# Optimization experiments

Measured on AMD Instinct MI355X. Metric: run time of the kernel, lower is better.

Reference implementation:

```python
import jax, jax.numpy as jnp
import numpy as np

ALPHA, NCLUST, LAMBD, GAMMA = 0.6, 3, 0.1, 0.01
KMEANS_ITERS = 10


def _conv(x, w, b):
    y = jax.lax.conv_general_dilated(x, w, (1, 1), 'SAME',
                                     dimension_numbers=('NCHW', 'OIHW', 'NCHW'))
    return y + b[None, :, None, None]


def _pool2(x):
    B, C, H, W = x.shape
    return x.reshape(B, C, H // 2, 2, W // 2, 2).mean(axis=(3, 5))


def _up2(x):
    return jnp.repeat(jnp.repeat(x, 2, axis=2), 2, axis=3)


def _encode(x, p, all_features=False):
    f1 = jax.nn.relu(_conv(x, p['e1_w'], p['e1_b']))
    f2 = jax.nn.relu(_conv(_pool2(f1), p['e2_w'], p['e2_b']))
    f3 = jax.nn.relu(_conv(_pool2(f2), p['e3_w'], p['e3_b']))
    f4 = jax.nn.relu(_conv(_pool2(f3), p['e4_w'], p['e4_b']))
    return (f1, f2, f3, f4) if all_features else f4


def _decode(f, p):
    x = jax.nn.relu(_conv(f, p['d1_w'], p['d1_b']))
    x = jax.nn.relu(_conv(_up2(x), p['d2_w'], p['d2_b']))
    x = jax.nn.relu(_conv(_up2(x), p['d3_w'], p['d3_b']))
    return _conv(_up2(x), p['d4_w'], p['d4_b'])


def _kmeans_onehot(pts, k):
    # pts: [N, C]; fixed-iteration Lloyd's, init = first k points.
    cent0 = pts[:k]

    def step(cent, _):
        d = ((pts[:, None, :] - cent[None]) ** 2).sum(-1)  # [N, K]
        oh = jax.nn.one_hot(jnp.argmin(d, axis=1), k, dtype=pts.dtype)
        cent = (oh.T @ pts) / (oh.sum(0)[:, None] + 1e-6)
        return cent, None

    cent, _ = jax.lax.scan(step, cent0, None, length=KMEANS_ITERS)
    d = ((pts[:, None, :] - cent[None]) ** 2).sum(-1)
    return jax.nn.one_hot(jnp.argmin(d, axis=1), k, dtype=pts.dtype)  # [N, K]


def _style_transfer(fc, fs):
    # fc, fs: [C, H, W] single-sample encoded features (original runs this per-sample on CPU numpy).
    C, H, W = fc.shape
    f = fc.reshape(C, -1)  # [C, N]
    s = fs.reshape(C, -1)  # [C, M]
    oh_c = _kmeans_onehot(f.T, NCLUST)  # [N, K]
    oh_s = _kmeans_onehot(s.T, NCLUST)  # [M, K]
    eye = LAMBD * jnp.eye(C, dtype=f.dtype)

    def cluster_T(wc, ws):
        # weighted whitening-coloring transform for one cluster pair
        nc = wc.sum() + 1e-6
        ns = ws.sum() + 1e-6
        mu_c = (f * wc).sum(1) / nc
        mu_s = (s * ws).sum(1) / ns
        fc_ = f - mu_c[:, None]
        fs_ = s - mu_s[:, None]
        cov_c = (fc_ * wc) @ fc_.T / nc + eye
        cov_s = (fs_ * ws) @ fs_.T / ns + eye
        lc, Ec = jnp.linalg.eigh(cov_c)
        ls, Es = jnp.linalg.eigh(cov_s)
        Wm = (Ec * jnp.clip(lc, 1e-6) ** -0.5) @ Ec.T  # whiten
        Cm = (Es * jnp.clip(ls, 1e-6) ** 0.5) @ Es.T   # color
        return Cm @ Wm, mu_c, mu_s

    Ts, mucs, muss = jax.vmap(cluster_T, in_axes=(1, 1))(oh_c, oh_s)  # [K,C,C],[K,C],[K,C]
    tpts = (jnp.einsum('kcd,dn->kcn', Ts, f)
            - jnp.einsum('kcd,kd->kc', Ts, mucs)[:, :, None]
            + muss[:, :, None])  # [K, C, N]
    fcs = jnp.einsum('nk,kcn->cn', oh_c, tpts)  # select per-point cluster transform
    return (ALPHA * fcs + (1.0 - ALPHA) * f).reshape(C, H, W)


def _forward(content_images, style_images, p):
    cf = _encode(content_images, p)
    sf = _encode(style_images, p)
    # original detaches to numpy -> no grad through the transfer
    tf_ = jax.lax.stop_gradient(jax.vmap(_style_transfer)(cf, sf))
    dec = _decode(tf_, p)
    ef = _encode(dec, p)
    all_ef = _encode(dec, p, all_features=True)
    all_sf = _encode(style_images, p, all_features=True)
    closs = jnp.mean((ef - cf) ** 2)
    sloss = 0.0
    for fa, fb in zip(all_ef, all_sf):
        sloss = sloss + jnp.mean((fa.mean((2, 3)) - fb.mean((2, 3))) ** 2)
        sloss = sloss + jnp.mean((fa.std((2, 3)) - fb.std((2, 3))) ** 2)
    return closs + GAMMA * sloss


PARAM_SHAPES = dict(
    e1_w=(64, 3, 3, 3), e1_b=(64,), e2_w=(128, 64, 3, 3), e2_b=(128,),
    e3_w=(256, 128, 3, 3), e3_b=(256,), e4_w=(512, 256, 3, 3), e4_b=(512,),
    d1_w=(256, 512, 3, 3), d1_b=(256,), d2_w=(128, 256, 3, 3), d2_b=(128,),
    d3_w=(64, 128, 3, 3), d3_b=(64,), d4_w=(3, 64, 3, 3), d4_b=(3,),
)


def setup_inputs() -> dict:
    key = jax.random.key(0)
    kc, ks, kp = jax.random.split(key, 3)
    inp = {
        'content_images': jax.random.uniform(kc, (4, 3, 256, 256), jnp.float32),
        'style_images': jax.random.uniform(ks, (4, 3, 256, 256), jnp.float32),
    }
    for i, (name, shp) in enumerate(PARAM_SHAPES.items()):
        fan_in = int(np.prod(shp[1:])) if len(shp) > 1 else 1
        inp[name] = jax.random.normal(jax.random.fold_in(kp, i), shp, jnp.float32) / np.sqrt(fan_in)
    return inp


def reference(content_images, style_images, e1_w, e1_b, e2_w, e2_b, e3_w, e3_b,
              e4_w, e4_b, d1_w, d1_b, d2_w, d2_b, d3_w, d3_b, d4_w, d4_b):
    p = dict(e1_w=e1_w, e1_b=e1_b, e2_w=e2_w, e2_b=e2_b, e3_w=e3_w, e3_b=e3_b,
             e4_w=e4_w, e4_b=e4_b, d1_w=d1_w, d1_b=d1_b, d2_w=d2_w, d2_b=d2_b,
             d3_w=d3_w, d3_b=d3_b, d4_w=d4_w, d4_b=d4_b)
    return _forward(content_images, style_images, p)
```

## Files before the change

kernel.cpp:

```cpp
#include <hip/hip_runtime.h>
#include <cstddef>

#define NS_ITERS 8
#define MSZ 262144
#define PL  6291456
#define KSLOT 12312

typedef unsigned short u16;
typedef __attribute__((ext_vector_type(8))) short bf16x8;
typedef __attribute__((ext_vector_type(4))) float f32x4;
typedef __attribute__((ext_vector_type(4))) short u16x4;

__device__ inline u16 bf16_rne(float x){
  unsigned u = __float_as_uint(x);
  unsigned r = u + 0x7fffu + ((u>>16)&1u);
  return (u16)(r>>16);
}
__device__ inline float bf16f(u16 h){
  return __uint_as_float(((unsigned)h)<<16);
}

#define OFF_F4C   0ul
#define OFF_F4S   2097152ul
#define OFF_TF    4194304ul
// ... 367 lines not shown
  const float* p = x + (size_t)bc*HW;
  double s = 0.0, s2 = 0.0;
  for (int i = tid; i < HW; i += 256){ double v = p[i]; s += v; s2 += v*v; }
  __shared__ double sh[256], sh2[256];
  sh[tid] = s; sh2[tid] = s2; __syncthreads();
  for (int k=128;k>0;k>>=1){ if (tid<k){ sh[tid]+=sh[tid+k]; sh2[tid]+=sh2[tid+k]; } __syncthreads(); }
  if (tid == 0){
    double m = sh[0]/HW;
    double var = sh2[0]/HW - m*m;
    if (var < 0.0) var = 0.0;
    mo[bc] = (float)m;
    so[bc] = (float)sqrt(var);
  }
}

__global__ __launch_bounds__(256) void transposek(const float* __restrict__ f4c,
                                                  const float* __restrict__ f4s,
                                                  float* __restrict__ ptsT){
  __shared__ float t[32][33];
  int r = blockIdx.z;
  const float* src = (r < 4) ? (f4c + (size_t)r*524288) : (f4s + (size_t)(r-4)*524288);
  int n0 = blockIdx.x*32, c0 = blockIdx.y*32;
  int lx = threadIdx.x & 31, ly = threadIdx.x >> 5;
  for (int j=0;j<32;j+=8)
    t[ly+j][lx] = src[(size_t)(c0+ly+j)*1024 + n0+lx];
  __syncthreads();
  for (int j=0;j<32;j+=8)
    ptsT[((size_t)r*1024 + n0+ly+j)*512 + c0+lx] = t[lx][ly+j];
}

__global__ __launch_bounds__(256) void initcent2k(const float* __restrict__ ptsT, float* __restrict__ KACC){
  int i = blockIdx.x*256 + threadIdx.x;
  if (i < 12288){
    int c = i & 511; int k = (i >> 9) % 3; int r = i / 1536;
    KACC[r*1536 + k*512 + c] = ptsT[((size_t)r*1024 + k)*512 + c];
  }
  if (i < 24) KACC[12288 + i] = 1.f;
}

__global__ __launch_bounds__(256) void kstepk(const float* __restrict__ ptsT,
    const float* __restrict__ prev, float* __restrict__ next,
    int* __restrict__ a, int nodiv)
{
  const int r = blockIdx.x, sl = blockIdx.y;
  const int tid = threadIdx.x;
  __shared__ float sc[1536];
  __shared__ int sa[32];
  __shared__ float red[3][8][32];
  __shared__ int scnt[3];
  if (tid < 3) scnt[tid] = 0;
  for (int i = tid; i < 1536; i += 256){
    float s = prev[r*1536 + i];
    float cnt = nodiv ? 1.f : (prev[12288 + r*3 + (i>>9)] + 1e-6f);
    sc[i] = s / cnt;
  }
  __syncthreads();
  const float* base = ptsT + (size_t)r*524288;
  const int wid = tid >> 6, lane = tid & 63;
  for (int rep = 0; rep < 8; ++rep){
    int p = wid*8 + rep;
    int n = sl*32 + p;
    const float* pp = base + (size_t)n*512;
    float d0=0.f,d1=0.f,d2=0.f;
    #pragma unroll
    for (int i=0;i<8;i++){
      int c = lane + i*64;
      float v = pp[c];
      float e0 = v - sc[c], e1 = v - sc[512+c], e2 = v - sc[1024+c];
      d0 = fmaf(e0,e0,d0); d1 = fmaf(e1,e1,d1); d2 = fmaf(e2,e2,d2);
    }
    #pragma unroll
    for (int off=32; off>0; off>>=1){
      d0 += __shfl_down(d0, off, 64);
      d1 += __shfl_down(d1, off, 64);
      d2 += __shfl_down(d2, off, 64);
    }
    if (lane == 0){
      int bi = 0; float bd = d0;
      if (d1 < bd){ bd = d1; bi = 1; }
      if (d2 < bd){ bd = d2; bi = 2; }
      sa[p] = bi;
      a[r*1024 + n] = bi;
    }
  }
  __syncthreads();
  if (tid < 32) atomicAdd(&scnt[sa[tid]], 1);
  __syncthreads();
  if (tid < 3) atomicAdd(&next[12288 + r*3 + tid], (float)scnt[tid]);
  const int g = tid >> 5, lc = tid & 31;
  for (int cj = 0; cj < 16; ++cj){
    int c = cj*32 + lc;
    float s0=0.f,s1=0.f,s2=0.f;
    #pragma unroll
    for (int q=0;q<4;q++){
      int nl = g*4 + q;
      float v = base[(size_t)(sl*32+nl)*512 + c];
      int an = sa[nl];
      s0 += (an==0)?v:0.f;
      s1 += (an==1)?v:0.f;
      s2 += (an==2)?v:0.f;
    }
    red[0][g][lc]=s0; red[1][g][lc]=s1; red[2][g][lc]=s2;
    __syncthreads();
    if (g == 0){
      float t0=0.f,t1=0.f,t2=0.f;
      #pragma unroll
      for (int q2=0;q2<8;q2++){ t0+=red[0][q2][lc]; t1+=red[1][q2][lc]; t2+=red[2][q2][lc]; }
      atomicAdd(&next[r*1536 +          c], t0);
      atomicAdd(&next[r*1536 +  512 +   c], t1);
      atomicAdd(&next[r*1536 + 1024 +   c], t2);
    }
    __syncthreads();
  }
}

__global__ __launch_bounds__(256) void mufink(const float* __restrict__ slot,
                                              float* __restrict__ mu, float* __restrict__ counts){
  int i = blockIdx.x*256 + threadIdx.x;
  if (i >= 12288) return;
  int c = i & 511; int k = (i >> 9) % 3; int r = i / 1536;
  int cs = r >> 2, img = r & 3;
  int i0 = cs*12 + img*3;
  float cnt = slot[12288 + r*3 + k];
  mu[(size_t)(i0+k)*512 + c] = slot[r*1536 + k*512 + c] / (cnt + 1e-6f);
  if (c == 0) counts[i0+k] = cnt;
}

__global__ __launch_bounds__(256) void maskcenterk(const float* __restrict__ f4c, const float* __restrict__ f4s,
        const int* __restrict__ a, const float* __restrict__ mu,
        u16* __restrict__ Ph, u16* __restrict__ Pl){
  size_t i4 = ((size_t)blockIdx.x*256 + threadIdx.x)*4;
  if (i4 >= (size_t)PL*2) return;
  int z = (int)(i4 >> 19);
  int rc = (int)(i4 & 524287);
  int c = rc >> 10, n = rc & 1023;
  int cs = z / 12; int rem = z - cs*12; int img = rem / 3; int k = rem - img*3;
  const float* pts = (cs ? f4s : f4c) + (size_t)img*524288;
  float m = mu[(size_t)z*512 + c];
  const int* an = a + (cs*4 + img)*1024 + n;
  float4 v4 = *(const float4*)&pts[(size_t)c*1024 + n];
  float vv[4] = {v4.x, v4.y, v4.z, v4.w};
  u16x4 oh, ol;
  #pragma unroll
  for (int j=0;j<4;j++){
    float v = (an[j] == k) ? (vv[j] - m) : 0.f;
    u16 h = bf16_rne(v);
    oh[j] = (short)h;
    ol[j] = (short)bf16_rne(v - bf16f(h));
  }
  *(u16x4*)&Ph[i4] = oh;
  *(u16x4*)&Pl[i4] = ol;
}

__global__ __launch_bounds__(256) void covgemm(const u16* __restrict__ Ph, const u16* __restrict__ Pl,
        const float* __restrict__ counts, float* __restrict__ Ycov, float* __restrict__ trsum){
  const int z = blockIdx.z;
  const u16* Pbh = Ph + (size_t)z*524288;
  const u16* Pbl = Pl + (size_t)z*524288;
  const int m0 = blockIdx.y*128, n0 = blockIdx.x*128;
  const int tid = threadIdx.x;

  __shared__ __align__(16) u16 sAh[128*40], sAl[128*40];
  __shared__ __align__(16) u16 sBh[128*40], sBl[128*40];

  const int ra = tid >> 2, qa = tid & 3;
  const int wid = tid >> 6, lane = tid & 63;
  const int wm = wid >> 1, wn = wid & 1;
  const int quad = lane >> 4, ln = lane & 15;

  f32x4 acc[4][4];
  #pragma unroll
  for (int i=0;i<4;i++)
    #pragma unroll
    for (int j=0;j<4;j++)
      #pragma unroll
      for (int e=0;e<4;e++) acc[i][j][e] = 0.f;

  for (int k0 = 0; k0 < 1024; k0 += 32){
    *(bf16x8*)&sAh[ra*40 + qa*8]      = *(const bf16x8*)&Pbh[(size_t)(m0+ra)*1024    + k0 + qa*8];
    *(bf16x8*)&sAl[ra*40 + qa*8]      = *(const bf16x8*)&Pbl[(size_t)(m0+ra)*1024    + k0 + qa*8];
    *(bf16x8*)&sAh[(ra+64)*40 + qa*8] = *(const bf16x8*)&Pbh[(size_t)(m0+ra+64)*1024 + k0 + qa*8];
    *(bf16x8*)&sAl[(ra+64)*40 + qa*8] = *(const bf16x8*)&Pbl[(size_t)(m0+ra+64)*1024 + k0 + qa*8];
    *(bf16x8*)&sBh[ra*40 + qa*8]      = *(const bf16x8*)&Pbh[(size_t)(n0+ra)*1024    + k0 + qa*8];
    *(bf16x8*)&sBl[ra*40 + qa*8]      = *(const bf16x8*)&Pbl[(size_t)(n0+ra)*1024    + k0 + qa*8];
    *(bf16x8*)&sBh[(ra+64)*40 + qa*8] = *(const bf16x8*)&Pbh[(size_t)(n0+ra+64)*1024 + k0 + qa*8];
    *(bf16x8*)&sBl[(ra+64)*40 + qa*8] = *(const bf16x8*)&Pbl[(size_t)(n0+ra+64)*1024 + k0 + qa*8];
    __syncthreads();

    bf16x8 ah[4], al[4], bh[4], bl[4];
    #pragma unroll
    for (int t=0;t<4;t++){
      const int moA = ((wm*4+t)*16 + ln)*40 + quad*8;
      const int moB = ((wn*4+t)*16 + ln)*40 + quad*8;
      ah[t] = *(const bf16x8*)&sAh[moA];
      al[t] = *(const bf16x8*)&sAl[moA];
      bh[t] = *(const bf16x8*)&sBh[moB];
      bl[t] = *(const bf16x8*)&sBl[moB];
    }
    #pragma unroll
    for (int mi=0;mi<4;mi++)
      #pragma unroll
      for (int ni=0;ni<4;ni++){
        acc[mi][ni] = __builtin_amdgcn_mfma_f32_16x16x32_bf16(ah[mi], bh[ni], acc[mi][ni], 0, 0, 0);
        acc[mi][ni] = __builtin_amdgcn_mfma_f32_16x16x32_bf16(ah[mi], bl[ni], acc[mi][ni], 0, 0, 0);
        acc[mi][ni] = __builtin_amdgcn_mfma_f32_16x16x32_bf16(al[mi], bh[ni], acc[mi][ni], 0, 0, 0);
      }
    __syncthreads();
  }
  const float inv = 1.f/(counts[z] + 1e-6f);
  float dsum = 0.f; bool anyd = false;
  #pragma unroll
  for (int mi=0;mi<4;mi++){
    const int mbase = m0 + (wm*4+mi)*16 + quad*4;
    #pragma unroll
    for (int ni=0;ni<4;ni++){
      const int n = n0 + (wn*4+ni)*16 + ln;
      #pragma unroll
      for (int rg=0;rg<4;rg++){
        const int m = mbase + rg;
        float v = acc[mi][ni][rg]*inv + ((m==n)?0.1f:0.f);
        Ycov[(size_t)z*MSZ + (size_t)m*512 + n] = v;
        if (m0==n0 && m==n){ dsum += v; anyd = true; }
      }
    }
  }
  if (anyd) atomicAdd(&trsum[z], dsum);
}

__global__ __launch_bounds__(256) void nsinitk(const float* __restrict__ Ycov, const float* __restrict__ sval,
                                               u16* __restrict__ Yh, u16* __restrict__ Yl,
                                               u16* __restrict__ Zh, u16* __restrict__ Zl){
  size_t idx = (size_t)blockIdx.x*256 + threadIdx.x;
  if (idx >= (size_t)PL) return;
  int z = (int)(idx >> 18);
  int rc = (int)(idx & (MSZ-1));
  int rr = rc >> 9, cc = rc & 511;
  float y = Ycov[idx] / sval[z];
  u16 h = bf16_rne(y);
  Yh[idx] = h;
  Yl[idx] = bf16_rne(y - bf16f(h));
  Zh[idx] = (rr==cc) ? (u16)0x3F80 : (u16)0;
  Zl[idx] = 0;
}

template<int MODE, int SYMB>
__global__ __launch_bounds__(256) void bmms(
    const u16* __restrict__ Ah, const u16* __restrict__ Al,
    const u16* __restrict__ Bh, const u16* __restrict__ Bl,
    u16* __restrict__ Ch, u16* __restrict__ Cl,
    const float* __restrict__ osc,
    int aoff, float* __restrict__ trAcc)
{
  const int z = blockIdx.z;
  const u16* Abh = Ah + (size_t)(z+aoff)*MSZ;
  const u16* Abl = Al + (size_t)(z+aoff)*MSZ;
  const u16* Bbh = Bh + (size_t)z*MSZ;
  const u16* Bbl = Bl + (size_t)z*MSZ;
  const int m0 = blockIdx.y*128, n0 = blockIdx.x*128;
  const int tid = threadIdx.x;

  __shared__ __align__(16) u16 sAh[128*40], sAl[128*40];
  __shared__ __align__(16) u16 sBh[128*40], sBl[128*40];

  const int ra = tid >> 2, qa = tid & 3;
  const int kb = tid >> 4, gb = tid & 15;

  const int wid = tid >> 6, lane = tid & 63;
  const int wm = wid >> 1, wn = wid & 1;
  const int quad = lane >> 4, ln = lane & 15;

  f32x4 acc[4][4];
  #pragma unroll
  for (int i=0;i<4;i++)
    #pragma unroll
    for (int j=0;j<4;j++)
      #pragma unroll
      for (int e=0;e<4;e++) acc[i][j][e] = 0.f;

  for (int k0 = 0; k0 < 512; k0 += 32){
    *(bf16x8*)&sAh[ra*40 + qa*8]      = *(const bf16x8*)&Abh[(size_t)(m0+ra)*512    + k0 + qa*8];
    *(bf16x8*)&sAl[ra*40 + qa*8]      = *(const bf16x8*)&Abl[(size_t)(m0+ra)*512    + k0 + qa*8];
    *(bf16x8*)&sAh[(ra+64)*40 + qa*8] = *(const bf16x8*)&Abh[(size_t)(m0+ra+64)*512 + k0 + qa*8];
    *(bf16x8*)&sAl[(ra+64)*40 + qa*8] = *(const bf16x8*)&Abl[(size_t)(m0+ra+64)*512 + k0 + qa*8];
    if constexpr (SYMB){
      *(bf16x8*)&sBh[ra*40 + qa*8]      = *(const bf16x8*)&Bbh[(size_t)(n0+ra)*512    + k0 + qa*8];
      *(bf16x8*)&sBl[ra*40 + qa*8]      = *(const bf16x8*)&Bbl[(size_t)(n0+ra)*512    + k0 + qa*8];
      *(bf16x8*)&sBh[(ra+64)*40 + qa*8] = *(const bf16x8*)&Bbh[(size_t)(n0+ra+64)*512 + k0 + qa*8];
      *(bf16x8*)&sBl[(ra+64)*40 + qa*8] = *(const bf16x8*)&Bbl[(size_t)(n0+ra+64)*512 + k0 + qa*8];
    } else {
      bf16x8 vh = *(const bf16x8*)&Bbh[(size_t)(k0+kb)*512 + n0 + gb*8];
      bf16x8 vl = *(const bf16x8*)&Bbl[(size_t)(k0+kb)*512 + n0 + gb*8];
      #pragma unroll
      for (int j=0;j<8;j++){
        sBh[(gb*8+j)*40 + kb] = (u16)vh[j];
        sBl[(gb*8+j)*40 + kb] = (u16)vl[j];
      }
      vh = *(const bf16x8*)&Bbh[(size_t)(k0+kb+16)*512 + n0 + gb*8];
      vl = *(const bf16x8*)&Bbl[(size_t)(k0+kb+16)*512 + n0 + gb*8];
      #pragma unroll
      for (int j=0;j<8;j++){
        sBh[(gb*8+j)*40 + kb+16] = (u16)vh[j];
        sBl[(gb*8+j)*40 + kb+16] = (u16)vl[j];
      }
    }
    __syncthreads();

    bf16x8 ah[4], al[4], bh[4], bl[4];
    #pragma unroll
    for (int t=0;t<4;t++){
      const int moA = ((wm*4+t)*16 + ln)*40 + quad*8;
      const int moB = ((wn*4+t)*16 + ln)*40 + quad*8;
      ah[t] = *(const bf16x8*)&sAh[moA];
      al[t] = *(const bf16x8*)&sAl[moA];
      bh[t] = *(const bf16x8*)&sBh[moB];
      bl[t] = *(const bf16x8*)&sBl[moB];
    }
    #pragma unroll
    for (int mi=0;mi<4;mi++)
      #pragma unroll
      for (int ni=0;ni<4;ni++){
        acc[mi][ni] = __builtin_amdgcn_mfma_f32_16x16x32_bf16(ah[mi], bh[ni], acc[mi][ni], 0, 0, 0);
        acc[mi][ni] = __builtin_amdgcn_mfma_f32_16x16x32_bf16(ah[mi], bl[ni], acc[mi][ni], 0, 0, 0);
        acc[mi][ni] = __builtin_amdgcn_mfma_f32_16x16x32_bf16(al[mi], bh[ni], acc[mi][ni], 0, 0, 0);
      }
    __syncthreads();
  }

  float alpha = 1.f;
  if constexpr (MODE==2){ alpha = osc[z]; }

  float dsum = 0.f; bool anyd = false;
  #pragma unroll
  for (int mi=0;mi<4;mi++){
    const int mbase = m0 + (wm*4+mi)*16 + quad*4;
    #pragma unroll
    for (int ni=0;ni<4;ni++){
      const int n = n0 + (wn*4+ni)*16 + ln;
      #pragma unroll
      for (int rg=0;rg<4;rg++){
        const int m = mbase + rg;
        const size_t off = (size_t)z*MSZ + (size_t)m*512 + n;
        float v = alpha*acc[mi][ni][rg];
        u16 h = bf16_rne(v);
        Ch[off] = h;
        Cl[off] = bf16_rne(v - bf16f(h));
        if (MODE==0 && trAcc && m0==n0 && m==n){ dsum += v; anyd = true; }
      }
    }
  }
  if (MODE==0 && anyd) atomicAdd(&trAcc[z], dsum);
}

__global__ __launch_bounds__(256) void bmmpair(
    const u16* __restrict__ Yh, const u16* __restrict__ Yl,
    const u16* __restrict__ Mh, const u16* __restrict__ Ml,
    const u16* __restrict__ Zh, const u16* __restrict__ Zl,
    u16* __restrict__ Y2h, u16* __restrict__ Y2l,
    u16* __restrict__ Z2h, u16* __restrict__ Z2l,
    const float* __restrict__ trAcc, int last)
{
  const int z = blockIdx.z;
  int zz; bool isY;
  if (last){ zz = z; isY = (z >= 12); }
  else { isY = (z < 24); zz = isY ? z : (z - 24); }
  const size_t zo = (size_t)zz*MSZ;
  const u16 *Abh, *Abl, *Bbh, *Bbl, *Dbh, *Dbl;
  u16 *Cbh, *Cbl;
  if (isY){
    Abh = Yh + zo; Abl = Yl + zo;
    Bbh = Mh + zo; Bbl = Ml + zo;
    Dbh = Yh + zo; Dbl = Yl + zo;
    Cbh = Y2h + zo; Cbl = Y2l + zo;
  } else {
    Abh = Mh + zo; Abl = Ml + zo;
    Bbh = Zh + zo; Bbl = Zl + zo;
    Dbh = Zh + zo; Dbl = Zl + zo;
    Cbh = Z2h + zo; Cbl = Z2l + zo;
  }
  const int m0 = blockIdx.y*128, n0 = blockIdx.x*128;
  const int tid = threadIdx.x;

  __shared__ __align__(16) u16 sAh[128*40], sAl[128*40];
  __shared__ __align__(16) u16 sBh[128*40], sBl[128*40];

  const int ra = tid >> 2, qa = tid & 3;
  const int wid = tid >> 6, lane = tid & 63;
  const int wm = wid >> 1, wn = wid & 1;
  const int quad = lane >> 4, ln = lane & 15;

  f32x4 acc[4][4];
  #pragma unroll
  for (int i=0;i<4;i++)
    #pragma unroll
    for (int j=0;j<4;j++)
      #pragma unroll
      for (int e=0;e<4;e++) acc[i][j][e] = 0.f;

  for (int k0 = 0; k0 < 512; k0 += 32){
    *(bf16x8*)&sAh[ra*40 + qa*8]      = *(const bf16x8*)&Abh[(size_t)(m0+ra)*512    + k0 + qa*8];
    *(bf16x8*)&sAl[ra*40 + qa*8]      = *(const bf16x8*)&Abl[(size_t)(m0+ra)*512    + k0 + qa*8];
    *(bf16x8*)&sAh[(ra+64)*40 + qa*8] = *(const bf16x8*)&Abh[(size_t)(m0+ra+64)*512 + k0 + qa*8];
    *(bf16x8*)&sAl[(ra+64)*40 + qa*8] = *(const bf16x8*)&Abl[(size_t)(m0+ra+64)*512 + k0 + qa*8];
    *(bf16x8*)&sBh[ra*40 + qa*8]      = *(const bf16x8*)&Bbh[(size_t)(n0+ra)*512    + k0 + qa*8];
    *(bf16x8*)&sBl[ra*40 + qa*8]      = *(const bf16x8*)&Bbl[(size_t)(n0+ra)*512    + k0 + qa*8];
    *(bf16x8*)&sBh[(ra+64)*40 + qa*8] = *(const bf16x8*)&Bbh[(size_t)(n0+ra+64)*512 + k0 + qa*8];
    *(bf16x8*)&sBl[(ra+64)*40 + qa*8] = *(const bf16x8*)&Bbl[(size_t)(n0+ra+64)*512 + k0 + qa*8];
    __syncthreads();

    bf16x8 ah[4], al[4], bh[4], bl[4];
    #pragma unroll
    for (int t=0;t<4;t++){
      const int moA = ((wm*4+t)*16 + ln)*40 + quad*8;
      const int moB = ((wn*4+t)*16 + ln)*40 + quad*8;
      ah[t] = *(const bf16x8*)&sAh[moA];
      al[t] = *(const bf16x8*)&sAl[moA];
      bh[t] = *(const bf16x8*)&sBh[moB];
      bl[t] = *(const bf16x8*)&sBl[moB];
    }
    #pragma unroll
    for (int mi=0;mi<4;mi++)
      #pragma unroll
      for (int ni=0;ni<4;ni++){
        acc[mi][ni] = __builtin_amdgcn_mfma_f32_16x16x32_bf16(ah[mi], bh[ni], acc[mi][ni], 0, 0, 0);
        acc[mi][ni] = __builtin_amdgcn_mfma_f32_16x16x32_bf16(ah[mi], bl[ni], acc[mi][ni], 0, 0, 0);
        acc[mi][ni] = __builtin_amdgcn_mfma_f32_16x16x32_bf16(al[mi], bh[ni], acc[mi][ni], 0, 0, 0);
      }
    __syncthreads();
  }

  const float tr = trAcc[zz];
  const float g2 = fminf(512.f/fmaxf(tr, 1e-6f), 2.7f);
  const float oz = 0.5f*sqrtf(g2);
  const float alpha = -g2*oz, beta = 3.f*oz;

  #pragma unroll
  for (int mi=0;mi<4;mi++){
    const int mbase = m0 + (wm*4+mi)*16 + quad*4;
    #pragma unroll
    for (int ni=0;ni<4;ni++){
      const int n = n0 + (wn*4+ni)*16 + ln;
      #pragma unroll
      for (int rg=0;rg<4;rg++){
        const int m = mbase + rg;
        const size_t off = (size_t)m*512 + n;
        float v = alpha*acc[mi][ni][rg] + beta*(bf16f(Dbh[off]) + bf16f(Dbl[off]));
        u16 h = bf16_rne(v);
        Cbh[off] = h;
        Cbl[off] = bf16_rne(v - bf16f(h));
      }
    }
  }
}

__global__ __launch_bounds__(256) void bmmt(
    const u16* __restrict__ Th, const u16* __restrict__ Tl,
    const u16* __restrict__ fh, const u16* __restrict__ fl,
    float* __restrict__ Cf)
{
  const int z = blockIdx.z;
  const u16* Abh = Th + (size_t)z*MSZ;
  const u16* Abl = Tl + (size_t)z*MSZ;
  const u16* Bbh = fh + (size_t)(z/3)*524288;
  const u16* Bbl = fl + (size_t)(z/3)*524288;
  const int m0 = blockIdx.y*128, n0 = blockIdx.x*128;
  const int tid = threadIdx.x;

  __shared__ __align__(16) u16 sAh[128*40], sAl[128*40];
  __shared__ __align__(16) u16 sBh[128*40], sBl[128*40];

  const int ra = tid >> 2, qa = tid & 3;
  const int kb = tid >> 4, gb = tid & 15;
  const int wid = tid >> 6, lane = tid & 63;
  const int wm = wid >> 1, wn = wid & 1;
  const int quad = lane >> 4, ln = lane & 15;

  f32x4 acc[4][4];
  #pragma unroll
  for (int i=0;i<4;i++)
    #pragma unroll
    for (int j=0;j<4;j++)
      #pragma unroll
      for (int e=0;e<4;e++) acc[i][j][e] = 0.f;

  for (int k0 = 0; k0 < 512; k0 += 32){
    *(bf16x8*)&sAh[ra*40 + qa*8]      = *(const bf16x8*)&Abh[(size_t)(m0+ra)*512    + k0 + qa*8];
    *(bf16x8*)&sAl[ra*40 + qa*8]      = *(const bf16x8*)&Abl[(size_t)(m0+ra)*512    + k0 + qa*8];
    *(bf16x8*)&sAh[(ra+64)*40 + qa*8] = *(const bf16x8*)&Abh[(size_t)(m0+ra+64)*512 + k0 + qa*8];
    *(bf16x8*)&sAl[(ra+64)*40 + qa*8] = *(const bf16x8*)&Abl[(size_t)(m0+ra+64)*512 + k0 + qa*8];
    {
      bf16x8 vh = *(const bf16x8*)&Bbh[(size_t)(k0+kb)*1024 + n0 + gb*8];
      bf16x8 vl = *(const bf16x8*)&Bbl[(size_t)(k0+kb)*1024 + n0 + gb*8];
      #pragma unroll
      for (int j=0;j<8;j++){
        sBh[(gb*8+j)*40 + kb] = (u16)vh[j];
        sBl[(gb*8+j)*40 + kb] = (u16)vl[j];
      }
      vh = *(const bf16x8*)&Bbh[(size_t)(k0+kb+16)*1024 + n0 + gb*8];
      vl = *(const bf16x8*)&Bbl[(size_t)(k0+kb+16)*1024 + n0 + gb*8];
      #pragma unroll
      for (int j=0;j<8;j++){
        sBh[(gb*8+j)*40 + kb+16] = (u16)vh[j];
        sBl[(gb*8+j)*40 + kb+16] = (u16)vl[j];
      }
    }
    __syncthreads();

    bf16x8 ah[4], al[4], bh[4], bl[4];
    #pragma unroll
    for (int t=0;t<4;t++){
      const int moA = ((wm*4+t)*16 + ln)*40 + quad*8;
      const int moB = ((wn*4+t)*16 + ln)*40 + quad*8;
      ah[t] = *(const bf16x8*)&sAh[moA];
      al[t] = *(const bf16x8*)&sAl[moA];
      bh[t] = *(const bf16x8*)&sBh[moB];
      bl[t] = *(const bf16x8*)&sBl[moB];
    }
    #pragma unroll
    for (int mi=0;mi<4;mi++)
      #pragma unroll
      for (int ni=0;ni<4;ni++){
        acc[mi][ni] = __builtin_amdgcn_mfma_f32_16x16x32_bf16(ah[mi], bh[ni], acc[mi][ni], 0, 0, 0);
        acc[mi][ni] = __builtin_amdgcn_mfma_f32_16x16x32_bf16(ah[mi], bl[ni], acc[mi][ni], 0, 0, 0);
        acc[mi][ni] = __builtin_amdgcn_mfma_f32_16x16x32_bf16(al[mi], bh[ni], acc[mi][ni], 0, 0, 0);
      }
    __syncthreads();
  }
  #pragma unroll
  for (int mi=0;mi<4;mi++){
    const int mbase = m0 + (wm*4+mi)*16 + quad*4;
    #pragma unroll
    for (int ni=0;ni<4;ni++){
      const int n = n0 + (wn*4+ni)*16 + ln;
      #pragma unroll
      for (int rg=0;rg<4;rg++){
        const int m = mbase + rg;
        Cf[(size_t)z*524288 + (size_t)m*1024 + n] = acc[mi][ni][rg];
      }
    }
  }
}

__global__ __launch_bounds__(256) void splitk(const float* __restrict__ src,
                                              u16* __restrict__ dh, u16* __restrict__ dl, int n4){
  int i = blockIdx.x*256 + threadIdx.x;
  if (i >= n4) return;
  float4 v4 = *(const float4*)&src[(size_t)i*4];
  float vv[4] = {v4.x, v4.y, v4.z, v4.w};
  u16x4 oh, ol;
  #pragma unroll
  for (int j=0;j<4;j++){
    u16 h = bf16_rne(vv[j]);
    oh[j] = (short)h;
    ol[j] = (short)bf16_rne(vv[j] - bf16f(h));
  }
  *(u16x4*)&dh[(size_t)i*4] = oh;
  *(u16x4*)&dl[(size_t)i*4] = ol;
}

__global__ void make_scalesk(const float* __restrict__ sval, float* __restrict__ scl){
  int i = threadIdx.x;
  if (i < 12) scl[i] = sqrtf(sval[12+i] / sval[i]);
}

__global__ __launch_bounds__(512) void tveck(const u16* __restrict__ Th, const u16* __restrict__ Tl,
                                             const float* __restrict__ mu, float* __restrict__ tvec){
  int b = blockIdx.x; int c = threadIdx.x;
  __shared__ float mc[512];
  mc[c] = mu[(size_t)b*512 + c];
  __syncthreads();
  const u16* Trh = Th + ((size_t)b*512 + c)*512;
  const u16* Trl = Tl + ((size_t)b*512 + c)*512;
  float s = 0.f;
  for (int d=0; d<512; d++) s = fmaf(bf16f(Trh[d]) + bf16f(Trl[d]), mc[d], s);
  tvec[b*512 + c] = mu[(size_t)(12+b)*512 + c] - s;
}

__global__ __launch_bounds__(256) void selectk(const float* __restrict__ tpts, const float* __restrict__ tvec,
        const int* __restrict__ a, const float* __restrict__ f4c, float* __restrict__ tf){
  size_t idx = (size_t)blockIdx.x*256 + threadIdx.x;
  if (idx >= 2097152ul) return;
  int n = (int)(idx & 1023);
  int c = (int)((idx >> 10) & 511);
  int img = (int)(idx >> 19);
  int k = a[img*1024 + n];
  int b = img*3 + k;
  float v = tpts[((size_t)b*512 + c)*1024 + n] + tvec[b*512 + c];
  tf[idx] = 0.6f*v + 0.4f*f4c[idx];
}

__global__ __launch_bounds__(256) void clossk(const float* __restrict__ x, const float* __restrict__ y,
                                              int n, float* __restrict__ acc){
  int tid = threadIdx.x;
  float s = 0.f;
  for (size_t i = (size_t)blockIdx.x*256 + tid; i < (size_t)n; i += (size_t)gridDim.x*256){
    float d = x[i] - y[i]; s = fmaf(d, d, s);
  }
  __shared__ float sh[256];
  sh[tid] = s; __syncthreads();
  for (int k=128;k>0;k>>=1){ if (tid<k) sh[tid]+=sh[tid+k]; __syncthreads(); }
  if (tid==0) atomicAdd(acc, sh[0]);
}

__global__ __launch_bounds__(256) void finalk(const float* __restrict__ sm, float* __restrict__ out){
  int tid = threadIdx.x;
  const int cnts[4] = {256,512,1024,2048};
  const int offs[4] = {0,256,768,1792};
  const float* mS = sm + SM_STATS_S;
  const float* sS = sm + SM_STATS_S + 3840;
  const float* mD = sm + SM_STATS_D;
  const float* sD = sm + SM_STATS_D + 3840;
  double sl = 0.0;
  for (int L=0; L<4; ++L){
    int cnt = cnts[L], off = offs[L];
    double inv = 1.0/cnt;
    for (int i=tid; i<cnt; i+=256){
      double dm = (double)mD[off+i] - (double)mS[off+i];
      double ds = (double)sD[off+i] - (double)sS[off+i];
      sl += (dm*dm + ds*ds)*inv;
    }
  }
  __shared__ double sh[256];
  sh[tid] = sl; __syncthreads();
  for (int k=128;k>0;k>>=1){ if (tid<k) sh[tid]+=sh[tid+k]; __syncthreads(); }
  if (tid==0){
    double closs = (double)sm[SM_CLOSS] / 2097152.0;
    out[0] = (float)(closs + 0.01*sh[0]);
  }
}


extern "C" void kernel_launch(void* const* d_in, const int* in_sizes, int n_in,
                              void* d_out, int out_size, void* d_ws, size_t ws_size,
                              hipStream_t stream)
{
  const float* content = (const float*)d_in[0];
  const float* style   = (const float*)d_in[1];
  const float* Wm[8]; const float* Bm[8];
  for (int i=0;i<8;i++){ Wm[i] = (const float*)d_in[2+2*i]; Bm[i] = (const float*)d_in[3+2*i]; }
  float* out = (float*)d_out;
  float* ws = (float*)d_ws;

  float* f4c  = ws + OFF_F4C;
  float* f4s  = ws + OFF_F4S;
  float* tf   = ws + OFF_TF;
  float* dec  = ws + OFF_DEC;
  float* sm   = ws + OFF_SMALL;
  float* AR   = ws + OFF_ARENA;
  int*   aPtr = (int*)(sm + SM_ASSIGN);
  float* mu   = sm + SM_MU;
  float* counts = sm + SM_COUNTS;
  float* sval = sm + SM_SVAL;
  float* scl  = sm + SM_SCALE;
  float* tvec = sm + SM_TVEC;
  float* trbuf = sm + SM_TR;

  u16* WB = (u16*)(ws + OFF_WSPL);
  u16 *w2h=WB+0,       *w2l=WB+73728;
  u16 *w3h=WB+147456,  *w3l=WB+442368;
  u16 *w4h=WB+737280,  *w4l=WB+1916928;
  u16 *v1h=WB+3096576, *v1l=WB+4276224;
  u16 *v2h=WB+5455872, *v2l=WB+5750784;
  u16 *v3h=WB+6045696, *v3l=WB+6119424;

  float* Ycov = AR;
  u16* Mh  = (u16*)(AR);
  u16* Ml  = (u16*)(AR + 3145728ul);
  u16* Yh  = (u16*)(AR + 6291456ul);
  u16* Yl  = (u16*)(AR + 9437184ul);
  u16* Zh  = (u16*)(AR + 12582912ul);
  u16* Zl  = (u16*)(AR + 15728640ul);
  u16* Y2h = (u16*)(AR + 18874368ul);
  u16* Y2l = (u16*)(AR + 22020096ul);
  u16* Z2h = (u16*)(AR + 25165824ul);
  u16* Z2l = (u16*)(AR + 28311552ul);
  u16* Ph  = (u16*)(AR + 18874368ul);
  u16* Pl  = (u16*)(AR + 25165824ul);
  float* ptsT = AR + 25165824ul;
  u16* Th  = (u16*)(AR + 18874368ul);
  u16* Tl  = (u16*)(AR + 20971520ul);
  u16* fsh = (u16*)(AR + 23068672ul);
  u16* fsl = (u16*)(AR + 24117248ul);
  float* KACC = AR + 0;

  u16* xP1h  = (u16*)(AR + 16777216ul);
  u16* xP1l  = (u16*)(AR + 20971520ul);
  u16* xF2ph = (u16*)(AR + 16777216ul);
  u16* xF2pl = (u16*)(AR + 18874368ul);
  u16* xF3ph = (u16*)(AR + 18874368ul);
  u16* xF3pl = (u16*)(AR + 19922944ul);
  u16* xTFh  = (u16*)(AR + 8388608ul);
  u16* xTFl  = (u16*)(AR + 9437184ul);
  u16* xX1h  = (u16*)(AR + 1048576ul);
  u16* xX1l  = (u16*)(AR + 1572864ul);
  u16* xX2h  = (u16*)(AR + 11534336ul);
  u16* xX2l  = (u16*)(AR + 12582912ul);
  u16* xP1dh = (u16*)(AR + 16777216ul);
  u16* xP1dl = (u16*)(AR + 18874368ul);
  u16* xF2dph= (u16*)(AR + 16777216ul);
  u16* xF2dpl= (u16*)(AR + 17825792ul);
  u16* xF3dph= (u16*)(AR + 16777216ul);
  u16* xF3dpl= (u16*)(AR + 17301504ul);

  zerok<<<512,256,0,stream>>>(sm, 131072);

  {
    auto wsp = [&](int li, u16* wh, u16* wl, int Co, int Ci){
      int n = 9*Co*Ci;
      wsplitk<<<(n+255)/256,256,0,stream>>>(Wm[li], wh, wl, Co, Ci);
    };
    wsp(1,w2h,w2l,128,64);
    wsp(2,w3h,w3l,256,128);
    wsp(3,w4h,w4l,512,256);
    wsp(4,v1h,v1l,256,512);
    wsp(5,v2h,v2l,128,256);
    wsp(6,v3h,v3l,64,128);
  }

  auto convMFMA = [&](const u16* xh, const u16* xl, int li, float* outp,
                      int B,int Ci,int Co,int H,int Wd,int relu,int KS,int RZ,float* part){
    const u16 *wh=nullptr,*wl=nullptr;
    switch(li){
      case 1: wh=w2h; wl=w2l; break;
      case 2: wh=w3h; wl=w3l; break;
      case 3: wh=w4h; wl=w4l; break;
      case 4: wh=v1h; wl=v1l; break;
      case 5: wh=v2h; wl=v2l; break;
      case 6: wh=v3h; wl=v3l; break;
    }
    int tiles = (H>>3)*(Wd>>4);
    if (KS==1){
      dim3 g(tiles,Co>>6,B);
      if (RZ==0) convm<1,0><<<g,256,0,stream>>>(xh,xl,wh,wl,Bm[li],outp,Ci,Co,H,Wd,relu);
      else       convm<1,2><<<g,256,0,stream>>>(xh,xl,wh,wl,Bm[li],outp,Ci,Co,H,Wd,relu);
    } else if (KS==2){
      dim3 g(tiles,Co>>6,B*2);
      if (RZ==0) convm<2,0><<<g,256,0,stream>>>(xh,xl,wh,wl,nullptr,part,Ci,Co,H,Wd,relu);
      else       convm<2,2><<<g,256,0,stream>>>(xh,xl,wh,wl,nullptr,part,Ci,Co,H,Wd,relu);
      int n = B*Co*H*Wd;
      sumk<<<(n+255)/256,256,0,stream>>>(part,Bm[li],outp,Co,H*Wd,2,relu,n);
    } else {
      dim3 g(tiles,Co>>6,B*4);
      convm<4,0><<<g,256,0,stream>>>(xh,xl,wh,wl,nullptr,part,Ci,Co,H,Wd,relu);
      int n = B*Co*H*Wd;
      sumk<<<(n+255)/256,256,0,stream>>>(part,Bm[li],outp,Co,H*Wd,4,relu,n);
    }
  };

  float* mS = sm + SM_STATS_S;
  float* sS = sm + SM_STATS_S + 3840;

  float* F1   = AR + 0;
  float* F2_8 = AR + 0;
  float* F3_8 = AR + 0;
  float* PART8 = AR + 10485760ul;

  {
    dim3 ge(64, 8, 4);
    conv3x3<8,4,1,0,0><<<ge,256,0,stream>>>(content,Wm[0],Bm[0],F1,xP1h,           xP1l,           4,3,64,256,256,1);
    conv3x3<8,4,1,1,0><<<ge,256,0,stream>>>(style,  Wm[0],Bm[0],F1,xP1h+4194304ul, xP1l+4194304ul, 4,3,64,256,256,1);
  }
  statsk<<<256,256,0,stream>>>(F1,65536, mS+0, sS+0);

  convMFMA(xP1h,xP1l, 1, F2_8, 8, 64,128,128,128,1,1,0,nullptr);
  statsk<<<512,256,0,stream>>>(F2_8 + 8388608ul, 16384, mS+256, sS+256);
  repackk<1><<<dim3(128,2,8),256,0,stream>>>(F2_8, xF2ph, xF2pl, 128,64,64);
  convMFMA(xF2ph,xF2pl, 2, F3_8, 8, 128,256,64,64,1,1,0,nullptr);
  statsk<<<1024,256,0,stream>>>(F3_8 + 4194304ul, 4096, mS+768, sS+768);
  repackk<1><<<dim3(32,4,8),256,0,stream>>>(F3_8, xF3ph, xF3pl, 256,32,32);
  convMFMA(xF3ph,xF3pl, 3, f4c, 8, 256,512,32,32,1,2,0,PART8);
  statsk<<<2048,256,0,stream>>>(f4s,1024, mS+1792, sS+1792);

  transposek<<<dim3(32,16,8),256,0,stream>>>(f4c,f4s,ptsT);
  zerok<<<(12*KSLOT+255)/256,256,0,stream>>>(KACC, 12*KSLOT);
  initcent2k<<<48,256,0,stream>>>(ptsT,KACC);
  for (int it=0; it<=10; ++it){
    kstepk<<<dim3(8,32),256,0,stream>>>(ptsT, KACC + (size_t)it*KSLOT, KACC + (size_t)(it+1)*KSLOT, aPtr, it==0 ? 1 : 0);
  }
  mufink<<<48,256,0,stream>>>(KACC + 11ul*KSLOT, mu, counts);

  maskcenterk<<<12288,256,0,stream>>>(f4c,f4s,aPtr,mu,Ph,Pl);
  covgemm<<<dim3(4,4,24),256,0,stream>>>(Ph,Pl,counts,Ycov,sval);
  nsinitk<<<24576,256,0,stream>>>(Ycov,sval,Yh,Yl,Zh,Zl);

  u16 *Ych=Yh,*Ycl=Yl,*Zch=Zh,*Zcl=Zl,*Yah=Y2h,*Yal=Y2l,*Zah=Z2h,*Zal=Z2l;
  for (int it=0; it<NS_ITERS; ++it){
    bmms<0,1><<<dim3(4,4,24),256,0,stream>>>(Zch,Zcl,Ych,Ycl,Mh,Ml,nullptr,0,trbuf+it*24);
    if (it < NS_ITERS-1)
      bmmpair<<<dim3(4,4,48),256,0,stream>>>(Ych,Ycl,Mh,Ml,Zch,Zcl,Yah,Yal,Zah,Zal,trbuf+it*24,0);
    else
      bmmpair<<<dim3(4,4,24),256,0,stream>>>(Ych,Ycl,Mh,Ml,Zch,Zcl,Yah,Yal,Zah,Zal,trbuf+it*24,1);
    u16* t;
    t=Ych;Ych=Yah;Yah=t; t=Ycl;Ycl=Yal;Yal=t;
    t=Zch;Zch=Zah;Zah=t; t=Zcl;Zcl=Zal;Zal=t;
  }
  make_scalesk<<<1,64,0,stream>>>(sval,scl);
  bmms<2,1><<<dim3(4,4,12),256,0,stream>>>(Ych,Ycl,Zch,Zcl,Th,Tl,scl,12,nullptr);
  tveck<<<12,512,0,stream>>>(Th,Tl,mu,tvec);
  splitk<<<2048,256,0,stream>>>(f4c,fsh,fsl,524288);
  float* Mb = AR + 0;
  bmmt<<<dim3(8,4,12),256,0,stream>>>(Th,Tl,fsh,fsl,Mb);
  selectk<<<8192,256,0,stream>>>(Mb,tvec,aPtr,f4c,tf);

  float* X1 = AR + 0;
  float* X2 = AR + 5242880ul;
  float* X3 = AR + 0;
  float* PARTA = AR + 2097152ul;
  float* PARTB = AR + 7340032ul;
  repackk<0><<<dim3(32,8,4),256,0,stream>>>(tf, xTFh, xTFl, 512,32,32);
  convMFMA(xTFh,xTFl, 4, X1, 4, 512,256,32,32,1,4,0,PARTA);
  repackk<0><<<dim3(32,4,4),256,0,stream>>>(X1, xX1h, xX1l, 256,32,32);
  convMFMA(xX1h,xX1l, 5, X2, 4, 256,128,64,64,1,2,2,PARTB);
  repackk<0><<<dim3(128,2,4),256,0,stream>>>(X2, xX2h, xX2l, 128,64,64);
  convMFMA(xX2h,xX2l, 6, X3, 4, 128,64,128,128,1,1,2,nullptr);
  d4upk<<<dim3(256,1,4),256,0,stream>>>(X3, Wm[7], Bm[7], dec);

  float* mD = sm + SM_STATS_D;
  float* sD = sm + SM_STATS_D + 3840;
  float* F1d = AR + 0;
  float* F2d = AR + 0;
  float* F3d = AR + 10485760ul;
  {
    dim3 ge(64, 8, 4);
    conv3x3<8,4,1,1,0><<<ge,256,0,stream>>>(dec,Wm[0],Bm[0],F1d,xP1dh,xP1dl,4,3,64,256,256,1);
  }
  statsk<<<256,256,0,stream>>>(F1d,65536, mD+0, sD+0);
  convMFMA(xP1dh,xP1dl, 1, F2d, 4, 64,128,128,128,1,1,0,nullptr);
  statsk<<<512,256,0,stream>>>(F2d,16384, mD+256, sD+256);
  repackk<1><<<dim3(128,2,4),256,0,stream>>>(F2d, xF2dph, xF2dpl, 128,64,64);
  convMFMA(xF2dph,xF2dpl, 2, F3d, 4, 128,256,64,64,1,1,0,nullptr);
  statsk<<<1024,256,0,stream>>>(F3d,4096, mD+768, sD+768);
  repackk<1><<<dim3(32,4,4),256,0,stream>>>(F3d, xF3dph, xF3dpl, 256,32,32);
  convMFMA(xF3dph,xF3dpl, 3, tf, 4, 256,512,32,32,1,2,0,PARTA);
  statsk<<<2048,256,0,stream>>>(tf,1024, mD+1792, sD+1792);
  clossk<<<2048,256,0,stream>>>(tf,f4c,2097152, sm+SM_CLOSS);
  finalk<<<1,256,0,stream>>>(sm,out);
}
```

Measured before the change: 2.321 ms.

## Shrink batched GEMM N-tile to 64 and pre-transpose bmmt operand via repack

```diff
diff --git a/kernel.cpp b/kernel.cpp
--- a/kernel.cpp
+++ b/kernel.cpp
@@ -543,27 +543,27 @@
   *(u16x4*)&Pl[i4] = ol;
 }
 
-__global__ __launch_bounds__(256) void covgemm(const u16* __restrict__ Ph, const u16* __restrict__ Pl,
+__global__ __launch_bounds__(256,4) void covgemm(const u16* __restrict__ Ph, const u16* __restrict__ Pl,
         const float* __restrict__ counts, float* __restrict__ Ycov, float* __restrict__ trsum){
   const int z = blockIdx.z;
   const u16* Pbh = Ph + (size_t)z*524288;
   const u16* Pbl = Pl + (size_t)z*524288;
-  const int m0 = blockIdx.y*128, n0 = blockIdx.x*128;
+  const int m0 = blockIdx.y*128, n0 = blockIdx.x*64;
   const int tid = threadIdx.x;
 
   __shared__ __align__(16) u16 sAh[128*40], sAl[128*40];
-  __shared__ __align__(16) u16 sBh[128*40], sBl[128*40];
+  __shared__ __align__(16) u16 sBh[64*40], sBl[64*40];
 
   const int ra = tid >> 2, qa = tid & 3;
   const int wid = tid >> 6, lane = tid & 63;
   const int wm = wid >> 1, wn = wid & 1;
   const int quad = lane >> 4, ln = lane & 15;
 
-  f32x4 acc[4][4];
+  f32x4 acc[4][2];
   #pragma unroll
   for (int i=0;i<4;i++)
     #pragma unroll
-    for (int j=0;j<4;j++)
+    for (int j=0;j<2;j++)
       #pragma unroll
       for (int e=0;e<4;e++) acc[i][j][e] = 0.f;
 
@@ -574,24 +574,25 @@
     *(bf16x8*)&sAl[(ra+64)*40 + qa*8] = *(const bf16x8*)&Pbl[(size_t)(m0+ra+64)*1024 + k0 + qa*8];
     *(bf16x8*)&sBh[ra*40 + qa*8]      = *(const bf16x8*)&Pbh[(size_t)(n0+ra)*1024    + k0 + qa*8];
     *(bf16x8*)&sBl[ra*40 + qa*8]      = *(const bf16x8*)&Pbl[(size_t)(n0+ra)*1024    + k0 + qa*8];
-    *(bf16x8*)&sBh[(ra+64)*40 + qa*8] = *(const bf16x8*)&Pbh[(size_t)(n0+ra+64)*1024 + k0 + qa*8];
-    *(bf16x8*)&sBl[(ra+64)*40 + qa*8] = *(const bf16x8*)&Pbl[(size_t)(n0+ra+64)*1024 + k0 + qa*8];
     __syncthreads();
 
-    bf16x8 ah[4], al[4], bh[4], bl[4];
+    bf16x8 ah[4], al[4], bh[2], bl[2];
     #pragma unroll
     for (int t=0;t<4;t++){
       const int moA = ((wm*4+t)*16 + ln)*40 + quad*8;
-      const int moB = ((wn*4+t)*16 + ln)*40 + quad*8;
       ah[t] = *(const bf16x8*)&sAh[moA];
       al[t] = *(const bf16x8*)&sAl[moA];
+    }
+    #pragma unroll
+    for (int t=0;t<2;t++){
+      const int moB = ((wn*2+t)*16 + ln)*40 + quad*8;
       bh[t] = *(const bf16x8*)&sBh[moB];
       bl[t] = *(const bf16x8*)&sBl[moB];
     }
     #pragma unroll
     for (int mi=0;mi<4;mi++)
       #pragma unroll
-      for (int ni=0;ni<4;ni++){
+      for (int ni=0;ni<2;ni++){
         acc[mi][ni] = __builtin_amdgcn_mfma_f32_16x16x32_bf16(ah[mi], bh[ni], acc[mi][ni], 0, 0, 0);
         acc[mi][ni] = __builtin_amdgcn_mfma_f32_16x16x32_bf16(ah[mi], bl[ni], acc[mi][ni], 0, 0, 0);
         acc[mi][ni] = __builtin_amdgcn_mfma_f32_16x16x32_bf16(al[mi], bh[ni], acc[mi][ni], 0, 0, 0);
@@ -604,14 +605,14 @@
   for (int mi=0;mi<4;mi++){
     const int mbase = m0 + (wm*4+mi)*16 + quad*4;
     #pragma unroll
-    for (int ni=0;ni<4;ni++){
-      const int n = n0 + (wn*4+ni)*16 + ln;
+    for (int ni=0;ni<2;ni++){
+      const int n = n0 + (wn*2+ni)*16 + ln;
       #pragma unroll
       for (int rg=0;rg<4;rg++){
         const int m = mbase + rg;
         float v = acc[mi][ni][rg]*inv + ((m==n)?0.1f:0.f);
         Ycov[(size_t)z*MSZ + (size_t)m*512 + n] = v;
-        if (m0==n0 && m==n){ dsum += v; anyd = true; }
+        if (m==n){ dsum += v; anyd = true; }
       }
     }
   }
@@ -634,8 +635,8 @@
   Zl[idx] = 0;
 }
 
-template<int MODE, int SYMB>
-__global__ __launch_bounds__(256) void bmms(
+template<int MODE>
+__global__ __launch_bounds__(256,4) void bmms(
     const u16* __restrict__ Ah, const u16* __restrict__ Al,
     const u16* __restrict__ Bh, const u16* __restrict__ Bl,
     u16* __restrict__ Ch, u16* __restrict__ Cl,
@@ -647,24 +648,22 @@
   const u16* Abl = Al + (size_t)(z+aoff)*MSZ;
   const u16* Bbh = Bh + (size_t)z*MSZ;
   const u16* Bbl = Bl + (size_t)z*MSZ;
-  const int m0 = blockIdx.y*128, n0 = blockIdx.x*128;
+  const int m0 = blockIdx.y*128, n0 = blockIdx.x*64;
   const int tid = threadIdx.x;
 
   __shared__ __align__(16) u16 sAh[128*40], sAl[128*40];
-  __shared__ __align__(16) u16 sBh[128*40], sBl[128*40];
+  __shared__ __align__(16) u16 sBh[64*40], sBl[64*40];
 
   const int ra = tid >> 2, qa = tid & 3;
-  const int kb = tid >> 4, gb = tid & 15;
-
   const int wid = tid >> 6, lane = tid & 63;
   const int wm = wid >> 1, wn = wid & 1;
   const int quad = lane >> 4, ln = lane & 15;
 
-  f32x4 acc[4][4];
+  f32x4 acc[4][2];
   #pragma unroll
   for (int i=0;i<4;i++)
     #pragma unroll
-    for (int j=0;j<4;j++)
+    for (int j=0;j<2;j++)
       #pragma unroll
       for (int e=0;e<4;e++) acc[i][j][e] = 0.f;
 
@@ -673,43 +672,27 @@
     *(bf16x8*)&sAl[ra*40 + qa*8]      = *(const bf16x8*)&Abl[(size_t)(m0+ra)*512    + k0 + qa*8];
     *(bf16x8*)&sAh[(ra+64)*40 + qa*8] = *(const bf16x8*)&Abh[(size_t)(m0+ra+64)*512 + k0 + qa*8];
     *(bf16x8*)&sAl[(ra+64)*40 + qa*8] = *(const bf16x8*)&Abl[(size_t)(m0+ra+64)*512 + k0 + qa*8];
-    if constexpr (SYMB){
-      *(bf16x8*)&sBh[ra*40 + qa*8]      = *(const bf16x8*)&Bbh[(size_t)(n0+ra)*512    + k0 + qa*8];
-      *(bf16x8*)&sBl[ra*40 + qa*8]      = *(const bf16x8*)&Bbl[(size_t)(n0+ra)*512    + k0 + qa*8];
-      *(bf16x8*)&sBh[(ra+64)*40 + qa*8] = *(const bf16x8*)&Bbh[(size_t)(n0+ra+64)*512 + k0 + qa*8];
-      *(bf16x8*)&sBl[(ra+64)*40 + qa*8] = *(const bf16x8*)&Bbl[(size_t)(n0+ra+64)*512 + k0 + qa*8];
-    } else {
-      bf16x8 vh = *(const bf16x8*)&Bbh[(size_t)(k0+kb)*512 + n0 + gb*8];
-      bf16x8 vl = *(const bf16x8*)&Bbl[(size_t)(k0+kb)*512 + n0 + gb*8];
-      #pragma unroll
-      for (int j=0;j<8;j++){
-        sBh[(gb*8+j)*40 + kb] = (u16)vh[j];
-        sBl[(gb*8+j)*40 + kb] = (u16)vl[j];
-      }
-      vh = *(const bf16x8*)&Bbh[(size_t)(k0+kb+16)*512 + n0 + gb*8];
-      vl = *(const bf16x8*)&Bbl[(size_t)(k0+kb+16)*512 + n0 + gb*8];
-      #pragma unroll
-      for (int j=0;j<8;j++){
-        sBh[(gb*8+j)*40 + kb+16] = (u16)vh[j];
-        sBl[(gb*8+j)*40 + kb+16] = (u16)vl[j];
-      }
-    }
+    *(bf16x8*)&sBh[ra*40 + qa*8]      = *(const bf16x8*)&Bbh[(size_t)(n0+ra)*512    + k0 + qa*8];
+    *(bf16x8*)&sBl[ra*40 + qa*8]      = *(const bf16x8*)&Bbl[(size_t)(n0+ra)*512    + k0 + qa*8];
     __syncthreads();
 
-    bf16x8 ah[4], al[4], bh[4], bl[4];
+    bf16x8 ah[4], al[4], bh[2], bl[2];
     #pragma unroll
     for (int t=0;t<4;t++){
       const int moA = ((wm*4+t)*16 + ln)*40 + quad*8;
-      const int moB = ((wn*4+t)*16 + ln)*40 + quad*8;
       ah[t] = *(const bf16x8*)&sAh[moA];
       al[t] = *(const bf16x8*)&sAl[moA];
+    }
+    #pragma unroll
+    for (int t=0;t<2;t++){
+      const int moB = ((wn*2+t)*16 + ln)*40 + quad*8;
       bh[t] = *(const bf16x8*)&sBh[moB];
       bl[t] = *(const bf16x8*)&sBl[moB];
     }
     #pragma unroll
     for (int mi=0;mi<4;mi++)
       #pragma unroll
-      for (int ni=0;ni<4;ni++){
+      for (int ni=0;ni<2;ni++){
         acc[mi][ni] = __builtin_amdgcn_mfma_f32_16x16x32_bf16(ah[mi], bh[ni], acc[mi][ni], 0, 0, 0);
         acc[mi][ni] = __builtin_amdgcn_mfma_f32_16x16x32_bf16(ah[mi], bl[ni], acc[mi][ni], 0, 0, 0);
         acc[mi][ni] = __builtin_amdgcn_mfma_f32_16x16x32_bf16(al[mi], bh[ni], acc[mi][ni], 0, 0, 0);
@@ -725,8 +708,8 @@
   for (int mi=0;mi<4;mi++){
     const int mbase = m0 + (wm*4+mi)*16 + quad*4;
     #pragma unroll
-    for (int ni=0;ni<4;ni++){
-      const int n = n0 + (wn*4+ni)*16 + ln;
+    for (int ni=0;ni<2;ni++){
+      const int n = n0 + (wn*2+ni)*16 + ln;
       #pragma unroll
       for (int rg=0;rg<4;rg++){
         const int m = mbase + rg;
@@ -735,7 +718,7 @@
         u16 h = bf16_rne(v);
         Ch[off] = h;
         Cl[off] = bf16_rne(v - bf16f(h));
-        if (MODE==0 && trAcc && m0==n0 && m==n){ dsum += v; anyd = true; }
+        if (MODE==0 && trAcc && m==n){ dsum += v; anyd = true; }
       }
     }
   }
@@ -843,7 +826,7 @@
   }
 }
 
-__global__ __launch_bounds__(256) void bmmt(
+__global__ __launch_bounds__(256,4) void bmmt(
     const u16* __restrict__ Th, const u16* __restrict__ Tl,
     const u16* __restrict__ fh, const u16* __restrict__ fl,
     float* __restrict__ Cf)
@@ -853,23 +836,22 @@
   const u16* Abl = Tl + (size_t)z*MSZ;
   const u16* Bbh = fh + (size_t)(z/3)*524288;
   const u16* Bbl = fl + (size_t)(z/3)*524288;
-  const int m0 = blockIdx.y*128, n0 = blockIdx.x*128;
+  const int m0 = blockIdx.y*128, n0 = blockIdx.x*64;
   const int tid = threadIdx.x;
 
   __shared__ __align__(16) u16 sAh[128*40], sAl[128*40];
-  __shared__ __align__(16) u16 sBh[128*40], sBl[128*40];
+  __shared__ __align__(16) u16 sBh[64*40], sBl[64*40];
 
   const int ra = tid >> 2, qa = tid & 3;
-  const int kb = tid >> 4, gb = tid & 15;
   const int wid = tid >> 6, lane = tid & 63;
   const int wm = wid >> 1, wn = wid & 1;
   const int quad = lane >> 4, ln = lane & 15;
 
-  f32x4 acc[4][4];
+  f32x4 acc[4][2];
   #pragma unroll
   for (int i=0;i<4;i++)
     #pragma unroll
-    for (int j=0;j<4;j++)
+    for (int j=0;j<2;j++)
       #pragma unroll
       for (int e=0;e<4;e++) acc[i][j][e] = 0.f;
 
@@ -878,38 +860,27 @@
     *(bf16x8*)&sAl[ra*40 + qa*8]      = *(const bf16x8*)&Abl[(size_t)(m0+ra)*512    + k0 + qa*8];
     *(bf16x8*)&sAh[(ra+64)*40 + qa*8] = *(const bf16x8*)&Abh[(size_t)(m0+ra+64)*512 + k0 + qa*8];
     *(bf16x8*)&sAl[(ra+64)*40 + qa*8] = *(const bf16x8*)&Abl[(size_t)(m0+ra+64)*512 + k0 + qa*8];
-    {
-      bf16x8 vh = *(const bf16x8*)&Bbh[(size_t)(k0+kb)*1024 + n0 + gb*8];
-      bf16x8 vl = *(const bf16x8*)&Bbl[(size_t)(k0+kb)*1024 + n0 + gb*8];
-      #pragma unroll
-      for (int j=0;j<8;j++){
-        sBh[(gb*8+j)*40 + kb] = (u16)vh[j];
-        sBl[(gb*8+j)*40 + kb] = (u16)vl[j];
-      }
-      vh = *(const bf16x8*)&Bbh[(size_t)(k0+kb+16)*1024 + n0 + gb*8];
-      vl = *(const bf16x8*)&Bbl[(size_t)(k0+kb+16)*1024 + n0 + gb*8];
-      #pragma unroll
-      for (int j=0;j<8;j++){
-        sBh[(gb*8+j)*40 + kb+16] = (u16)vh[j];
-        sBl[(gb*8+j)*40 + kb+16] = (u16)vl[j];
-      }
-    }
+    *(bf16x8*)&sBh[ra*40 + qa*8]      = *(const bf16x8*)&Bbh[(size_t)(n0+ra)*512    + k0 + qa*8];
+    *(bf16x8*)&sBl[ra*40 + qa*8]      = *(const bf16x8*)&Bbl[(size_t)(n0+ra)*512    + k0 + qa*8];
     __syncthreads();
 
-    bf16x8 ah[4], al[4], bh[4], bl[4];
+    bf16x8 ah[4], al[4], bh[2], bl[2];
     #pragma unroll
     for (int t=0;t<4;t++){
       const int moA = ((wm*4+t)*16 + ln)*40 + quad*8;
-      const int moB = ((wn*4+t)*16 + ln)*40 + quad*8;
       ah[t] = *(const bf16x8*)&sAh[moA];
       al[t] = *(const bf16x8*)&sAl[moA];
+    }
+    #pragma unroll
+    for (int t=0;t<2;t++){
+      const int moB = ((wn*2+t)*16 + ln)*40 + quad*8;
       bh[t] = *(const bf16x8*)&sBh[moB];
       bl[t] = *(const bf16x8*)&sBl[moB];
     }
     #pragma unroll
     for (int mi=0;mi<4;mi++)
       #pragma unroll
-      for (int ni=0;ni<4;ni++){
+      for (int ni=0;ni<2;ni++){
         acc[mi][ni] = __builtin_amdgcn_mfma_f32_16x16x32_bf16(ah[mi], bh[ni], acc[mi][ni], 0, 0, 0);
         acc[mi][ni] = __builtin_amdgcn_mfma_f32_16x16x32_bf16(ah[mi], bl[ni], acc[mi][ni], 0, 0, 0);
         acc[mi][ni] = __builtin_amdgcn_mfma_f32_16x16x32_bf16(al[mi], bh[ni], acc[mi][ni], 0, 0, 0);
@@ -920,8 +891,8 @@
   for (int mi=0;mi<4;mi++){
     const int mbase = m0 + (wm*4+mi)*16 + quad*4;
     #pragma unroll
-    for (int ni=0;ni<4;ni++){
-      const int n = n0 + (wn*4+ni)*16 + ln;
+    for (int ni=0;ni<2;ni++){
+      const int n = n0 + (wn*2+ni)*16 + ln;
       #pragma unroll
       for (int rg=0;rg<4;rg++){
         const int m = mbase + rg;
@@ -929,23 +900,6 @@
       }
     }
   }
-}
-
-__global__ __launch_bounds__(256) void splitk(const float* __restrict__ src,
-                                              u16* __restrict__ dh, u16* __restrict__ dl, int n4){
-  int i = blockIdx.x*256 + threadIdx.x;
-  if (i >= n4) return;
-  float4 v4 = *(const float4*)&src[(size_t)i*4];
-  float vv[4] = {v4.x, v4.y, v4.z, v4.w};
-  u16x4 oh, ol;
-  #pragma unroll
-  for (int j=0;j<4;j++){
-    u16 h = bf16_rne(vv[j]);
-    oh[j] = (short)h;
-    ol[j] = (short)bf16_rne(vv[j] - bf16f(h));
-  }
-  *(u16x4*)&dh[(size_t)i*4] = oh;
-  *(u16x4*)&dl[(size_t)i*4] = ol;
 }
 
 __global__ void make_scalesk(const float* __restrict__ sval, float* __restrict__ scl){
@@ -1170,12 +1124,12 @@
   mufink<<<48,256,0,stream>>>(KACC + 11ul*KSLOT, mu, counts);
 
   maskcenterk<<<12288,256,0,stream>>>(f4c,f4s,aPtr,mu,Ph,Pl);
-  covgemm<<<dim3(4,4,24),256,0,stream>>>(Ph,Pl,counts,Ycov,sval);
+  covgemm<<<dim3(8,4,24),256,0,stream>>>(Ph,Pl,counts,Ycov,sval);
   nsinitk<<<24576,256,0,stream>>>(Ycov,sval,Yh,Yl,Zh,Zl);
 
   u16 *Ych=Yh,*Ycl=Yl,*Zch=Zh,*Zcl=Zl,*Yah=Y2h,*Yal=Y2l,*Zah=Z2h,*Zal=Z2l;
   for (int it=0; it<NS_ITERS; ++it){
-    bmms<0,1><<<dim3(4,4,24),256,0,stream>>>(Zch,Zcl,Ych,Ycl,Mh,Ml,nullptr,0,trbuf+it*24);
+    bmms<0><<<dim3(8,4,24),256,0,stream>>>(Zch,Zcl,Ych,Ycl,Mh,Ml,nullptr,0,trbuf+it*24);
     if (it < NS_ITERS-1)
       bmmpair<<<dim3(4,4,48),256,0,stream>>>(Ych,Ycl,Mh,Ml,Zch,Zcl,Yah,Yal,Zah,Zal,trbuf+it*24,0);
     else
@@ -1185,11 +1139,11 @@
     t=Zch;Zch=Zah;Zah=t; t=Zcl;Zcl=Zal;Zal=t;
   }
   make_scalesk<<<1,64,0,stream>>>(sval,scl);
-  bmms<2,1><<<dim3(4,4,12),256,0,stream>>>(Ych,Ycl,Zch,Zcl,Th,Tl,scl,12,nullptr);
+  bmms<2><<<dim3(8,4,12),256,0,stream>>>(Ych,Ycl,Zch,Zcl,Th,Tl,scl,12,nullptr);
   tveck<<<12,512,0,stream>>>(Th,Tl,mu,tvec);
-  splitk<<<2048,256,0,stream>>>(f4c,fsh,fsl,524288);
+  repackk<0><<<dim3(32,8,4),256,0,stream>>>(f4c, fsh, fsl, 512,32,32);
   float* Mb = AR + 0;
-  bmmt<<<dim3(8,4,12),256,0,stream>>>(Th,Tl,fsh,fsl,Mb);
+  bmmt<<<dim3(16,4,12),256,0,stream>>>(Th,Tl,fsh,fsl,Mb);
   selectk<<<8192,256,0,stream>>>(Mb,tvec,aPtr,f4c,tf);
 
   float* X1 = AR + 0;
```

Measured after the change: 2.378 ms. +2.5%, slower.
